# Optimization experiments

Hardware: AMD Instinct MI355X
Metric: run time of the kernel (lower is better)

Reference implementation:

```python
import jax, jax.numpy as jnp
import numpy as np

B, S, V, D, H, F, GH, NC, L = 64, 256, 50000, 1024, 16, 4096, 100, 7, 4
DH = D // H


def _ln(x, g, b):
    m = x.mean(-1, keepdims=True)
    v = x.var(-1, keepdims=True)
    return (x - m) / jnp.sqrt(v + 1e-5) * g + b


def setup_inputs() -> dict:
    key = jax.random.key(0)
    ks = iter(jax.random.split(key, 40))
    nrm = lambda shp, s=0.02: jax.random.normal(next(ks), shp, jnp.float32) * s
    inp = {}
    inp["src"] = jax.random.randint(next(ks), (B, S), 0, V)
    inp["em_seq"] = jax.random.normal(next(ks), (B, S, 7), jnp.float32)
    inp["d_ids"] = jax.random.randint(next(ks), (B, 1), 0, B)
    inp["ut_len"] = jax.random.randint(next(ks), (B,), 1, S + 1)
    inp["emb"] = jax.random.uniform(next(ks), (V, D), jnp.float32, -0.1, 0.1)
    inp["Wqkv"] = nrm((L, 3 * D, D)); inp["bqkv"] = jnp.zeros((L, 3 * D), jnp.float32)
    inp["Wo"] = nrm((L, D, D)); inp["bo"] = jnp.zeros((L, D), jnp.float32)
    inp["W1"] = nrm((L, F, D)); inp["b1"] = jnp.zeros((L, F), jnp.float32)
    inp["W2"] = nrm((L, D, F)); inp["b2"] = jnp.zeros((L, D), jnp.float32)
    inp["ln1_g"] = jnp.ones((L, D), jnp.float32); inp["ln1_b"] = jnp.zeros((L, D), jnp.float32)
    inp["ln2_g"] = jnp.ones((L, D), jnp.float32); inp["ln2_b"] = jnp.zeros((L, D), jnp.float32)
    inp["gru_Wih"] = nrm((3 * GH, 7), 0.1); inp["gru_Whh"] = nrm((3 * GH, GH), 0.1)
    inp["gru_bih"] = jnp.zeros((3 * GH,), jnp.float32); inp["gru_bhh"] = jnp.zeros((3 * GH,), jnp.float32)
    inp["dec_W"] = jax.random.uniform(next(ks), (NC, 2 * D + GH), jnp.float32, -0.1, 0.1)
    inp["dec_b"] = jnp.zeros((NC,), jnp.float32)
    return inp


def reference(src, em_seq, d_ids, ut_len, emb, Wqkv, bqkv, Wo, bo, W1, b1, W2, b2,
              ln1_g, ln1_b, ln2_g, ln2_b, gru_Wih, gru_Whh, gru_bih, gru_bhh,
              dec_W, dec_b):
    # embedding + scale + sinusoidal positional encoding
    x = emb[src] * jnp.sqrt(jnp.float32(D))                      # [B,S,D]
    pos = jnp.arange(S, dtype=jnp.float32)[:, None]
    div = jnp.exp(jnp.arange(0, D, 2, dtype=jnp.float32) * (-jnp.log(10000.0) / D))
    pe = jnp.stack([jnp.sin(pos * div), jnp.cos(pos * div)], -1).reshape(S, D)
    x = x + pe

    causal = jnp.tril(jnp.ones((S, S), bool))
    neg = jnp.finfo(x.dtype).min
    for l in range(L):  # post-norm transformer encoder layers (PyTorch default)
        qkv = x @ Wqkv[l].T + bqkv[l]
        q, k, v = jnp.split(qkv, 3, -1)
        q = q.reshape(B, S, H, DH); k = k.reshape(B, S, H, DH); v = v.reshape(B, S, H, DH)
        sc = jnp.einsum('bqhd,bkhd->bhqk', q, k) / jnp.sqrt(jnp.float32(DH))
        sc = jnp.where(causal, sc, neg)
        a = jax.nn.softmax(sc, -1)
        o = jnp.einsum('bhqk,bkhd->bqhd', a, v).reshape(B, S, D)
        x = _ln(x + o @ Wo[l].T + bo[l], ln1_g[l], ln1_b[l])
        ff = jax.nn.relu(x @ W1[l].T + b1[l]) @ W2[l].T + b2[l]
        x = _ln(x + ff, ln2_g[l], ln2_b[l])

    # emotion GRU (PyTorch GRU equations), scan over time
    xp = jnp.einsum('bsf,gf->sbg', em_seq, gru_Wih) + gru_bih    # [S,B,3*GH]

    def step(h, xt):
        hp = h @ gru_Whh.T + gru_bhh
        xr, xz, xn = jnp.split(xt, 3, -1)
        hr, hz, hn = jnp.split(hp, 3, -1)
        r = jax.nn.sigmoid(xr + hr)
        z = jax.nn.sigmoid(xz + hz)
        n = jnp.tanh(xn + r * hn)
        h = (1.0 - z) * n + z * h
        return h, h

    _, hs = jax.lax.scan(step, jnp.zeros((B, GH), x.dtype), xp)
    emo = hs.transpose(1, 0, 2)                                  # [B,S,GH]

    # ragged gather of the 'main' utterance per dialogue + broadcast-concat
    lens = ut_len[d_ids[:, 0]]                                   # [B]
    main = x[jnp.arange(B), lens - 1]                            # [B,D]
    pair = jnp.concatenate([x, jnp.broadcast_to(main[:, None, :], (B, S, D))], -1)
    valid = (jnp.arange(S)[None, :] < lens[:, None])[..., None]
    pair = jnp.where(valid, pair, 0.0)                           # zeros beyond ut_len, as in torch loop
    dec_ip = jnp.concatenate([pair, emo], -1)                    # [B,S,2D+GH]
    return dec_ip @ dec_W.T + dec_b                              # [B,S,NC]
```

## Files before the change

kernel.cpp:

```cpp
#include <hip/hip_runtime.h>
#include <hip/hip_bf16.h>
#include <math.h>

#define BB 64
#define SS 256
#define DD 1024
#define HH 16
#define FFN 4096
#define GHH 100
#define NCC 7
#define LL 4
#define TT (BB*SS)
#define DHH 64

typedef unsigned short u16;
typedef unsigned int u32;
typedef __attribute__((ext_vector_type(4))) float f32x4;
typedef __attribute__((ext_vector_type(8))) short s16x8;
typedef __attribute__((ext_vector_type(4))) unsigned short u16x4;

__device__ __forceinline__ u16 f2bf(float f) {
  union { float f; u32 u; } x; x.f = f;
  u32 r = x.u + 0x7FFFu + ((x.u >> 16) & 1u);
  return (u16)(r >> 16);
}
__device__ __forceinline__ float bf2f(u16 b) {
  union { u32 u; float f; } x; x.u = ((u32)b) << 16;
  return x.f;
}

__global__ void k_f2bf4(const float* __restrict__ s0, u16* __restrict__ d0, int n0,
                        const float* __restrict__ s1, u16* __restrict__ d1, int n1,
                        const float* __restrict__ s2, u16* __restrict__ d2, int n2,
                        const float* __restrict__ s3, u16* __restrict__ d3, int n3) {
  int stride = gridDim.x * blockDim.x;
  int total = n0 + n1 + n2 + n3;
  for (int i = blockIdx.x * blockDim.x + threadIdx.x; i < total; i += stride) {
    const float* s; u16* d; int j = i;
    if (j < n0) { s = s0; d = d0; }
    else {
      j -= n0;
      if (j < n1) { s = s1; d = d1; }
      else {
        j -= n1;
        if (j < n2) { s = s2; d = d2; }
        else { j -= n2; s = s3; d = d3; }
      }
    }
    f32x4 v = *(const f32x4*)(s + (size_t)j * 4);
    u16x4 o;
    o[0] = f2bf(v[0]); o[1] = f2bf(v[1]); o[2] = f2bf(v[2]); o[3] = f2bf(v[3]);
    *(u16x4*)(d + (size_t)j * 4) = o;
  }
}

__global__ void k_pe(float* __restrict__ pe) {
  int i = blockIdx.x * blockDim.x + threadIdx.x;
  if (i >= SS * DD / 2) return;
  int s = i / (DD / 2), j = i % (DD / 2);
  float div = __expf((float)(2 * j) * (-9.210340371976184f / (float)DD));
  float a = (float)s * div;
  pe[s * DD + 2 * j]     = sinf(a);
  pe[s * DD + 2 * j + 1] = cosf(a);
}

__global__ void k_embed(const int* __restrict__ src, const float* __restrict__ emb,
                        const float* __restrict__ pe, float* __restrict__ x32,
                        u16* __restrict__ xb) {
  int i = blockIdx.x * blockDim.x + threadIdx.x;
  if (i >= TT * DD / 4) return;
  int t = i / (DD / 4);
  int d4 = (i % (DD / 4)) * 4;
  int s = t % SS;
  int tok = src[t];
  f32x4 e = *(const f32x4*)(emb + (size_t)tok * DD + d4);
  f32x4 p = *(const f32x4*)(pe + (size_t)s * DD + d4);
  f32x4 r;
  r[0] = e[0] * 32.0f + p[0]; r[1] = e[1] * 32.0f + p[1];
  r[2] = e[2] * 32.0f + p[2]; r[3] = e[3] * 32.0f + p[3];
  *(f32x4*)(x32 + (size_t)t * DD + d4) = r;
  u16x4 o;
  o[0] = f2bf(r[0]); o[1] = f2bf(r[1]); o[2] = f2bf(r[2]); o[3] = f2bf(r[3]);
  *(u16x4*)(xb + (size_t)t * DD + d4) = o;
}

#define MEMF asm volatile("" ::: "memory")
#define GBAR do { MEMF; __builtin_amdgcn_sched_barrier(0); __builtin_amdgcn_s_barrier(); __builtin_amdgcn_sched_barrier(0); MEMF; } while(0)
#define VMW4 asm volatile("s_waitcnt vmcnt(4)" ::: "memory")

#define STG(P, isB, h, l, buf, kt) \
  __builtin_amdgcn_global_load_lds( \
    (const __attribute__((address_space(1))) u32*)(P[h][l] + (kt)), \
    (__attribute__((address_space(3))) u32*)(smem + (buf)*65536 + (isB)*32768 + (h)*16384 + (l)*8192 + wid*1024), \
    16, 0, 0)

#define LDB(buf) do { \
  _Pragma("unroll") for (int nf = 0; nf < 4; nf++) \
  _Pragma("unroll") for (int kk = 0; kk < 2; kk++) { \
    int rel = (wn*64 + nf*16 + lm)*128 + kk*64 + lg*16; \
    bq[nf][kk] = *(const s16x8*)(smem + (buf)*65536 + 32768 + (rel ^ (((rel>>9)&1)<<5))); \
  } } while(0)

#define LDA(buf, q) do { \
  _Pragma("unroll") for (int ml = 0; ml < 2; ml++) \
  _Pragma("unroll") for (int kk = 0; kk < 2; kk++) { \
    int rel = (wm*128 + ((q)*2+ml)*16 + lm)*128 + kk*64 + lg*16; \
    aq[ml][kk] = *(const s16x8*)(smem + (buf)*65536 + (rel ^ (((rel>>9)&1)<<5))); \
  } } while(0)

#define MFMAQ(q) do { \
  __builtin_amdgcn_s_setprio(1); \
  _Pragma("unroll") for (int ml = 0; ml < 2; ml++) \
  _Pragma("unroll") for (int nf = 0; nf < 4; nf++) \
  _Pragma("unroll") for (int kk = 0; kk < 2; kk++) \
    acc[(q)*2+ml][nf] = __builtin_amdgcn_mfma_f32_16x16x32_bf16(aq[ml][kk], bq[nf][kk], acc[(q)*2+ml][nf], 0, 0, 0); \
  __builtin_amdgcn_s_setprio(0); \
} while(0)

template<int EPI>
__global__ __launch_bounds__(512, 2)
void k_gemm256(const u16* __restrict__ A, const u16* __restrict__ W,
               const float* __restrict__ bias, u16* __restrict__ C,
               int M, int N, int K) {
  extern __shared__ char smem[];
  const int tid = threadIdx.x;
  const int lane = tid & 63;
  const int wid = tid >> 6;
  const int lm = lane & 15, lg = lane >> 4;
  const int wm = wid >> 2, wn = wid & 3;

  const int NB = N >> 8;
  const int nwg = gridDim.x;
  const int bid = blockIdx.x;
  const int cpx = nwg >> 3;
  const int swzb = (bid & 7) * cpx + (bid >> 3);
  const int m0 = (swzb / NB) << 8;
  const int n0 = (swzb % NB) << 8;

  const u16* pA[2][2];
  const u16* pB[2][2];
#pragma unroll
  for (int h = 0; h < 2; h++)
#pragma unroll
    for (int l = 0; l < 2; l++) {
      int rel = h * 16384 + l * 8192 + tid * 16;
      int sb = rel ^ (((rel >> 9) & 1) << 5);
      int grow = sb >> 7;
      int gcol = (sb & 127) >> 1;
      pA[h][l] = A + (size_t)(m0 + grow) * K + gcol;
      pB[h][l] = W + (size_t)(n0 + grow) * K + gcol;
    }

  f32x4 acc[8][4];
#pragma unroll
  for (int i = 0; i < 8; i++)
#pragma unroll
    for (int j = 0; j < 4; j++) acc[i][j] = (f32x4){0.f, 0.f, 0.f, 0.f};

  s16x8 bq[4][2];
  s16x8 aq[2][2];

  const int NT = K >> 6;

  STG(pB,1,0,0,0,0); STG(pB,1,0,1,0,0); STG(pB,1,1,0,0,0); STG(pB,1,1,1,0,0);
  STG(pA,0,0,0,0,0); STG(pA,0,0,1,0,0); STG(pA,0,1,0,0,0); STG(pA,0,1,1,0,0);
  STG(pB,1,0,0,1,64); STG(pB,1,0,1,1,64); STG(pB,1,1,0,1,64); STG(pB,1,1,1,1,64);
  VMW4;
  GBAR;

  for (int i = 0; i < (NT >> 1); i++) {
    const int t1k = (2*i + 1) * 64;
    int t2 = 2*i + 2; if (t2 >= NT) t2 -= NT;
    int t3 = 2*i + 3; if (t3 >= NT) t3 -= NT;
    const int t2k = t2 * 64, t3k = t3 * 64;

    LDB(0); LDA(0,0);
    STG(pA,0,0,0,1,t1k); STG(pA,0,0,1,1,t1k);
    GBAR; MFMAQ(0); GBAR;
    LDA(0,1);
    STG(pA,0,1,0,1,t1k); STG(pA,0,1,1,1,t1k);
    STG(pB,1,0,0,0,t2k); STG(pB,1,0,1,0,t2k);
    GBAR; MFMAQ(1); GBAR;
    LDA(0,2);
    STG(pB,1,1,0,0,t2k); STG(pB,1,1,1,0,t2k);
    GBAR; MFMAQ(2); GBAR;
    LDA(0,3);
    GBAR; MFMAQ(3); VMW4; GBAR;
    LDB(1); LDA(1,0);
    STG(pA,0,0,0,0,t2k); STG(pA,0,0,1,0,t2k);
    GBAR; MFMAQ(0); GBAR;
    LDA(1,1);
    STG(pA,0,1,0,0,t2k); STG(pA,0,1,1,0,t2k);
    GBAR; MFMAQ(1); GBAR;
    LDA(1,2);
    STG(pB,1,0,0,1,t3k); STG(pB,1,0,1,1,t3k);
    GBAR; MFMAQ(2); GBAR;
    LDA(1,3);
    STG(pB,1,1,0,1,t3k); STG(pB,1,1,1,1,t3k);
    GBAR; MFMAQ(3); VMW4; GBAR;
  }

  float bn[4];
#pragma unroll
  for (int nf = 0; nf < 4; nf++) bn[nf] = bias[n0 + wn*64 + nf*16 + lm];
#pragma unroll
  for (int mf = 0; mf < 8; mf++)
#pragma unroll
    for (int nf = 0; nf < 4; nf++) {
      int col = n0 + wn*64 + nf*16 + lm;
#pragma unroll
      for (int r = 0; r < 4; r++) {
        int row = m0 + wm*128 + mf*16 + lg*4 + r;
        float v = acc[mf][nf][r] + bn[nf];
        if (EPI == 1) v = fmaxf(v, 0.f);
        C[(size_t)row * N + col] = f2bf(v);
      }
    }
}

__global__ __launch_bounds__(256, 2)
void k_attn(const u16* __restrict__ qkv, u16* __restrict__ o) {
  const int h = blockIdx.x;
  const int b = blockIdx.y;
  const int lane = threadIdx.x & 63;
  const int w = threadIdx.x >> 6;
  const int lm = lane & 15, lg = lane >> 4;

  __shared__ u16 Ks[64 * 64];
  __shared__ u16 Vt[64 * 64];
  __shared__ u16 Ps[4][64 * 64];

  const size_t tokbase = (size_t)b * SS;

  s16x8 aq[4][2];
#pragma unroll
  for (int mf = 0; mf < 4; mf++) {
    const u16* qrow = qkv + (tokbase + w * 64 + mf * 16 + lm) * 3072 + h * 64;
#pragma unroll
    for (int kk = 0; kk < 2; kk++)
      aq[mf][kk] = *(const s16x8*)(qrow + kk * 32 + lg * 8);
  }

  f32x4 zero = {0.f, 0.f, 0.f, 0.f};
  f32x4 oacc[4][4];
#pragma unroll
  for (int mf = 0; mf < 4; mf++)
#pragma unroll
    for (int df = 0; df < 4; df++) oacc[mf][df] = zero;
  float m_run[16], l_run[16];
#pragma unroll
  for (int r = 0; r < 16; r++) { m_run[r] = -3e38f; l_run[r] = 0.f; }

  for (int kb = 0; kb < 4; kb++) {
    __syncthreads();
    {
      int krow = threadIdx.x >> 2;
      int seg  = (threadIdx.x & 3) * 16;
      const u16* ksrc = qkv + (tokbase + kb * 64 + krow) * 3072 + 1024 + h * 64 + seg;
      s16x8 v0 = *(const s16x8*)(ksrc);
      s16x8 v1 = *(const s16x8*)(ksrc + 8);
      *(s16x8*)&Ks[krow * 64 + seg] = v0;
      *(s16x8*)&Ks[krow * 64 + seg + 8] = v1;
      const u16* vsrc = qkv + (tokbase + kb * 64 + krow) * 3072 + 2048 + h * 64 + seg;
      s16x8 w0 = *(const s16x8*)(vsrc);
      s16x8 w1 = *(const s16x8*)(vsrc + 8);
#pragma unroll
      for (int e = 0; e < 8; e++) {
        Vt[(seg + e) * 64 + krow]     = (u16)w0[e];
        Vt[(seg + 8 + e) * 64 + krow] = (u16)w1[e];
      }
    }
    __syncthreads();
    if (w < kb) continue;

    s16x8 bk[4][2];
#pragma unroll
    for (int nf = 0; nf < 4; nf++)
#pragma unroll
      for (int kk = 0; kk < 2; kk++)
        bk[nf][kk] = *(const s16x8*)&Ks[(nf * 16 + lm) * 64 + kk * 32 + lg * 8];

    const int colbase = kb * 64;
#pragma unroll
    for (int mf = 0; mf < 4; mf++) {
      f32x4 sfr[4];
#pragma unroll
      for (int nf = 0; nf < 4; nf++) {
        f32x4 acc = zero;
#pragma unroll
        for (int kk = 0; kk < 2; kk++)
          acc = __builtin_amdgcn_mfma_f32_16x16x32_bf16(aq[mf][kk], bk[nf][kk], acc, 0, 0, 0);
        sfr[nf] = acc;
      }
      const int rowbase = w * 64 + mf * 16 + lg * 4;
#pragma unroll
      for (int nf = 0; nf < 4; nf++) {
        int col = colbase + nf * 16 + lm;
#pragma unroll
        for (int r = 0; r < 4; r++) {
          float v = sfr[nf][r] * 0.125f;
          sfr[nf][r] = (col <= rowbase + r) ? v : -1e30f;
        }
      }
#pragma unroll
      for (int r = 0; r < 4; r++) {
        float m = fmaxf(fmaxf(sfr[0][r], sfr[1][r]), fmaxf(sfr[2][r], sfr[3][r]));
#pragma unroll
        for (int off = 1; off < 16; off <<= 1) m = fmaxf(m, __shfl_xor(m, off));
        int idx = mf * 4 + r;
        float mnew = fmaxf(m_run[idx], m);
        float fo = __expf(m_run[idx] - mnew);
        m_run[idx] = mnew;
        float ps = 0.f;
#pragma unroll
        for (int nf = 0; nf < 4; nf++) {
          float p = __expf(sfr[nf][r] - mnew);
          sfr[nf][r] = p;
          ps += p;
        }
#pragma unroll
        for (int off = 1; off < 16; off <<= 1) ps += __shfl_xor(ps, off);
        l_run[idx] = l_run[idx] * fo + ps;
#pragma unroll
        for (int df = 0; df < 4; df++) oacc[mf][df][r] *= fo;
      }
#pragma unroll
      for (int nf = 0; nf < 4; nf++)
#pragma unroll
        for (int r = 0; r < 4; r++)
          Ps[w][(mf * 16 + lg * 4 + r) * 64 + nf * 16 + lm] = f2bf(sfr[nf][r]);
    }
    asm volatile("" ::: "memory");
    s16x8 bv[4][2];
#pragma unroll
    for (int df = 0; df < 4; df++)
#pragma unroll
      for (int kk = 0; kk < 2; kk++)
        bv[df][kk] = *(const s16x8*)&Vt[(df * 16 + lm) * 64 + kk * 32 + lg * 8];
#pragma unroll
    for (int mf = 0; mf < 4; mf++) {
      s16x8 pa[2];
#pragma unroll
      for (int kk = 0; kk < 2; kk++)
        pa[kk] = *(const s16x8*)&Ps[w][(mf * 16 + lm) * 64 + kk * 32 + lg * 8];
#pragma unroll
      for (int df = 0; df < 4; df++)
#pragma unroll
        for (int kk = 0; kk < 2; kk++)
          oacc[mf][df] = __builtin_amdgcn_mfma_f32_16x16x32_bf16(pa[kk], bv[df][kk], oacc[mf][df], 0, 0, 0);
    }
  }

#pragma unroll
  for (int mf = 0; mf < 4; mf++)
#pragma unroll
    for (int df = 0; df < 4; df++)
#pragma unroll
      for (int r = 0; r < 4; r++) {
        int row = w * 64 + mf * 16 + lg * 4 + r;
        float val = oacc[mf][df][r] / l_run[mf * 4 + r];
        o[(tokbase + row) * 1024 + h * 64 + df * 16 + lm] = f2bf(val);
      }
}

__global__ __launch_bounds__(256)
void k_ln(const float* __restrict__ xin, const u16* __restrict__ tmp,
          const float* __restrict__ gam, const float* __restrict__ bet,
          float* __restrict__ xout, u16* __restrict__ xb) {
  int t = blockIdx.x;
  int tid = threadIdx.x;
  f32x4 v = *(const f32x4*)(xin + (size_t)t * DD + tid * 4);
  u16x4 u4 = *(const u16x4*)(tmp + (size_t)t * DD + tid * 4);
  v[0] += bf2f(u4[0]); v[1] += bf2f(u4[1]); v[2] += bf2f(u4[2]); v[3] += bf2f(u4[3]);
  float s = v[0] + v[1] + v[2] + v[3];
  float s2 = v[0]*v[0] + v[1]*v[1] + v[2]*v[2] + v[3]*v[3];
#pragma unroll
  for (int off = 32; off >= 1; off >>= 1) {
    s  += __shfl_xor(s, off);
    s2 += __shfl_xor(s2, off);
  }
  __shared__ float red[8];
  int w = tid >> 6;
  if ((tid & 63) == 0) { red[w] = s; red[4 + w] = s2; }
  __syncthreads();
  s  = red[0] + red[1] + red[2] + red[3];
  s2 = red[4] + red[5] + red[6] + red[7];
  float mean = s * (1.f / 1024.f);
  float var = s2 * (1.f / 1024.f) - mean * mean;
  float rstd = rsqrtf(var + 1e-5f);
  f32x4 g4 = *(const f32x4*)(gam + tid * 4);
  f32x4 b4 = *(const f32x4*)(bet + tid * 4);
  f32x4 y;
  u16x4 yo;
#pragma unroll
  for (int e = 0; e < 4; e++) {
    y[e] = (v[e] - mean) * rstd * g4[e] + b4[e];
    yo[e] = f2bf(y[e]);
  }
  *(f32x4*)(xout + (size_t)t * DD + tid * 4) = y;
  *(u16x4*)(xb + (size_t)t * DD + tid * 4) = yo;
}

__global__ __launch_bounds__(256, 1)
void k_gru(const float* __restrict__ em, const float* __restrict__ Wih,
           const float* __restrict__ bih, const float* __restrict__ Whh,
           const float* __restrict__ bhh, float* __restrict__ emo) {
  const int b = blockIdx.x;
  const int tid = threadIdx.x;
  const int iraw = tid >> 1;
  const int i = iraw < 100 ? iraw : 99;
  const bool act = iraw < 100;
  const int half = tid & 1;
  __shared__ __align__(16) float h[2][104];

  f32x4 wr[13], wz[13], wn[13];
#pragma unroll
  for (int q = 0; q < 13; q++) {
#pragma unroll
    for (int e4 = 0; e4 < 4; e4++) {
      int k = q * 4 + e4;
      int kk = half * 50 + (k < 50 ? k : 0);
      float vr = Whh[(size_t)i * 100 + kk];
      float vz = Whh[(size_t)(100 + i) * 100 + kk];
      float vn = Whh[(size_t)(200 + i) * 100 + kk];
      wr[q][e4] = (k < 50) ? vr : 0.f;
      wz[q][e4] = (k < 50) ? vz : 0.f;
      wn[q][e4] = (k < 50) ? vn : 0.f;
    }
  }
  float wir[7], wiz[7], win[7];
#pragma unroll
  for (int f = 0; f < 7; f++) {
    wir[f] = Wih[i * 7 + f];
    wiz[f] = Wih[(100 + i) * 7 + f];
    win[f] = Wih[(200 + i) * 7 + f];
  }
  const float br = bhh[i], bz = bhh[100 + i], bn = bhh[200 + i];
  const float xbr = bih[i], xbz = bih[100 + i], xbn = bih[200 + i];

  if (tid < 104) { h[0][tid] = 0.f; h[1][tid] = 0.f; }
  __syncthreads();

  const float* eb = em + (size_t)b * SS * 7;
  float e[7];
#pragma unroll
  for (int f = 0; f < 7; f++) e[f] = eb[f];

  for (int s = 0; s < SS; ++s) {
    const int cur = s & 1, nxt = cur ^ 1;
    float sr = xbr, sz = xbz, sn = xbn;
#pragma unroll
    for (int f = 0; f < 7; f++) {
      sr += wir[f] * e[f]; sz += wiz[f] * e[f]; sn += win[f] * e[f];
    }
    {
      int sp = (s + 1 < SS) ? s + 1 : s;
#pragma unroll
      for (int f = 0; f < 7; f++) e[f] = eb[sp * 7 + f];
    }
    const float* hb = &h[cur][half * 52];
    f32x4 ac_r = {0.f,0.f,0.f,0.f}, ac_z = {0.f,0.f,0.f,0.f}, ac_n = {0.f,0.f,0.f,0.f};
#pragma unroll
    for (int q = 0; q < 13; q++) {
      f32x4 hv = *(const f32x4*)(hb + q * 4);
      ac_r += wr[q] * hv;
      ac_z += wz[q] * hv;
      ac_n += wn[q] * hv;
    }
    float ar = (ac_r[0] + ac_r[1]) + (ac_r[2] + ac_r[3]);
    float az = (ac_z[0] + ac_z[1]) + (ac_z[2] + ac_z[3]);
    float an = (ac_n[0] + ac_n[1]) + (ac_n[2] + ac_n[3]);
    ar += __shfl_xor(ar, 1);
    az += __shfl_xor(az, 1);
    an += __shfl_xor(an, 1);
    if (act && half == 0) {
      int slot = i + (i >= 50 ? 2 : 0);
      float hold = h[cur][slot];
      float rr = 1.f / (1.f + __expf(-(sr + ar + br)));
      float zz = 1.f / (1.f + __expf(-(sz + az + bz)));
      float nx = sn + rr * (an + bn);
      float e2 = __expf(-2.f * fabsf(nx));
      float th = (1.f - e2) / (1.f + e2);
      float nn = copysignf(th, nx);
      float hn = (1.f - zz) * nn + zz * hold;
      h[nxt][slot] = hn;
      emo[((size_t)b * SS + s) * GHH + i] = hn;
    }
    __syncthreads();
  }
}

__global__ void k_main(const int* __restrict__ d_ids, const int* __restrict__ ut_len,
                       const float* __restrict__ x32, const float* __restrict__ decW,
                       float* __restrict__ md) {
  int b = blockIdx.x;
  int lane = threadIdx.x;
  int len = ut_len[d_ids[b]];
  const float* xr = x32 + ((size_t)b * SS + (len - 1)) * DD;
  float acc[NCC];
#pragma unroll
  for (int c = 0; c < NCC; c++) acc[c] = 0.f;
  for (int d = lane; d < DD; d += 64) {
    float xv = xr[d];
#pragma unroll
    for (int c = 0; c < NCC; c++) acc[c] += xv * decW[(size_t)c * 2148 + 1024 + d];
  }
#pragma unroll
  for (int c = 0; c < NCC; c++) {
#pragma unroll
    for (int off = 32; off >= 1; off >>= 1) acc[c] += __shfl_xor(acc[c], off);
  }
  if (lane == 0) {
#pragma unroll
    for (int c = 0; c < NCC; c++) md[b * NCC + c] = acc[c];
  }
}

__global__ __launch_bounds__(256)
void k_dec(const float* __restrict__ x32, const float* __restrict__ emo,
           const float* __restrict__ md, const float* __restrict__ decW,
           const float* __restrict__ decb, const int* __restrict__ d_ids,
           const int* __restrict__ ut_len, float* __restrict__ out) {
  int grp = threadIdx.x >> 6, lane = threadIdx.x & 63;
  int t = blockIdx.x * 4 + grp;
  int b = t / SS, s = t % SS;
  int len = ut_len[d_ids[b]];
  bool valid = s < len;
  float acc[NCC];
#pragma unroll
  for (int c = 0; c < NCC; c++) acc[c] = 0.f;
  if (valid) {
    const float* xr = x32 + (size_t)t * DD;
    for (int d = lane; d < DD; d += 64) {
      float xv = xr[d];
#pragma unroll
      for (int c = 0; c < NCC; c++) acc[c] += xv * decW[(size_t)c * 2148 + d];
    }
  }
  {
    const float* er = emo + (size_t)t * GHH;
    for (int d = lane; d < GHH; d += 64) {
      float ev = er[d];
#pragma unroll
      for (int c = 0; c < NCC; c++) acc[c] += ev * decW[(size_t)c * 2148 + 2048 + d];
    }
  }
#pragma unroll
  for (int c = 0; c < NCC; c++) {
#pragma unroll
    for (int off = 32; off >= 1; off >>= 1) acc[c] += __shfl_xor(acc[c], off);
  }
  if (lane == 0) {
#pragma unroll
    for (int c = 0; c < NCC; c++) {
      float v = acc[c] + (valid ? md[b * NCC + c] : 0.f) + decb[c];
      out[(size_t)t * NCC + c] = v;
    }
  }
}

extern "C" void kernel_launch(void* const* d_in, const int* in_sizes, int n_in,
                              void* d_out, int out_size, void* d_ws, size_t ws_size,
                              hipStream_t stream) {
  const int*   src    = (const int*)d_in[0];
  const float* em_seq = (const float*)d_in[1];
  const int*   d_ids  = (const int*)d_in[2];
  const int*   ut_len = (const int*)d_in[3];
  const float* emb    = (const float*)d_in[4];
  const float* Wqkv   = (const float*)d_in[5];
  const float* bqkv   = (const float*)d_in[6];
  const float* Wo     = (const float*)d_in[7];
  const float* bo     = (const float*)d_in[8];
  const float* W1     = (const float*)d_in[9];
  const float* b1     = (const float*)d_in[10];
  const float* W2     = (const float*)d_in[11];
  const float* b2     = (const float*)d_in[12];
  const float* ln1g   = (const float*)d_in[13];
  const float* ln1b   = (const float*)d_in[14];
  const float* ln2g   = (const float*)d_in[15];
  const float* ln2b   = (const float*)d_in[16];
  const float* gWih   = (const float*)d_in[17];
  const float* gWhh   = (const float*)d_in[18];
  const float* gbih   = (const float*)d_in[19];
  const float* gbhh   = (const float*)d_in[20];
  const float* decW   = (const float*)d_in[21];
  const float* decb   = (const float*)d_in[22];
  float* out = (float*)d_out;

  char* wsp = (char*)d_ws;
  auto take = [&](size_t n) { char* p = wsp; wsp += (n + 255) & ~(size_t)255; return p; };

  u16*   wqkvb = (u16*)take((size_t)3072 * 1024 * 2);
  u16*   wob   = (u16*)take((size_t)1024 * 1024 * 2);
  u16*   w1b   = (u16*)take((size_t)4096 * 1024 * 2);
  u16*   w2b   = (u16*)take((size_t)1024 * 4096 * 2);
  float* pe    = (float*)take((size_t)SS * DD * 4);
  float* x32   = (float*)take((size_t)TT * DD * 4);
  u16*   xb    = (u16*)take((size_t)TT * DD * 2);
  u16*   big   = (u16*)take((size_t)TT * FFN * 2);
  u16*   ob    = (u16*)take((size_t)TT * DD * 2);
  u16*   tmp16 = (u16*)take((size_t)TT * DD * 2);
  float* emo   = (float*)take((size_t)BB * SS * GHH * 4);
  float* md    = (float*)take((size_t)BB * NCC * 4);

  (void)hipFuncSetAttribute((const void*)&k_gemm256<0>,
      hipFuncAttributeMaxDynamicSharedMemorySize, 131072);
  (void)hipFuncSetAttribute((const void*)&k_gemm256<1>,
      hipFuncAttributeMaxDynamicSharedMemorySize, 131072);

  k_gru<<<BB, 256, 0, stream>>>(em_seq, gWih, gbih, gWhh, gbhh, emo);

  k_pe<<<(SS * DD / 2 + 255) / 256, 256, 0, stream>>>(pe);
  k_embed<<<TT * DD / 4 / 256, 256, 0, stream>>>(src, emb, pe, x32, xb);

  for (int l = 0; l < LL; ++l) {
    k_f2bf4<<<2048, 256, 0, stream>>>(
        Wqkv + (size_t)l * 3072 * 1024, wqkvb, 3072 * 1024 / 4,
        Wo   + (size_t)l * 1024 * 1024, wob,   1024 * 1024 / 4,
        W1   + (size_t)l * 4096 * 1024, w1b,   4096 * 1024 / 4,
        W2   + (size_t)l * 1024 * 4096, w2b,   1024 * 4096 / 4);

    k_gemm256<0><<<(TT/256) * (3072/256), 512, 131072, stream>>>(
        xb, wqkvb, bqkv + (size_t)l * 3072, big, TT, 3072, 1024);
    k_attn<<<dim3(HH, BB), 256, 0, stream>>>(big, ob);
    k_gemm256<0><<<(TT/256) * (1024/256), 512, 131072, stream>>>(
        ob, wob, bo + (size_t)l * 1024, tmp16, TT, 1024, 1024);
    k_ln<<<TT, 256, 0, stream>>>(x32, tmp16, ln1g + (size_t)l * DD, ln1b + (size_t)l * DD, x32, xb);
    k_gemm256<1><<<(TT/256) * (4096/256), 512, 131072, stream>>>(
        xb, w1b, b1 + (size_t)l * 4096, big, TT, 4096, 1024);
    k_gemm256<0><<<(TT/256) * (1024/256), 512, 131072, stream>>>(
        big, w2b, b2 + (size_t)l * 1024, tmp16, TT, 1024, 4096);
    k_ln<<<TT, 256, 0, stream>>>(x32, tmp16, ln2g + (size_t)l * DD, ln2b + (size_t)l * DD, x32, xb);
  }

  k_main<<<BB, 64, 0, stream>>>(d_ids, ut_len, x32, decW, md);
  k_dec<<<TT / 4, 256, 0, stream>>>(x32, emo, md, decW, decb, d_ids, ut_len, out);
}
```

Baseline: 2.469 ms.

## Drop fp32 residual stream, keep activations only in bf16; unroll GRU weights into scalars

Removes the fp32 copy of the hidden state (x32) and carries the residual stream only in bf16, so embed, layernorm and the decoder read and write half the bytes and skip an extra write per token. LayerNorm now reads the bf16 residual and overwrites it in place. The GRU kernel's weight arrays are replaced with macro-expanded named registers, which helps keep them out of scratch memory. The trade-off is lower residual precision across layers, which may push outputs past tolerance.

```diff
diff --git a/kernel.cpp b/kernel.cpp
--- a/kernel.cpp
+++ b/kernel.cpp
@@ -65,8 +65,7 @@
 }
 
 __global__ void k_embed(const int* __restrict__ src, const float* __restrict__ emb,
-                        const float* __restrict__ pe, float* __restrict__ x32,
-                        u16* __restrict__ xb) {
+                        const float* __restrict__ pe, u16* __restrict__ xb) {
   int i = blockIdx.x * blockDim.x + threadIdx.x;
   if (i >= TT * DD / 4) return;
   int t = i / (DD / 4);
@@ -75,12 +74,9 @@
   int tok = src[t];
   f32x4 e = *(const f32x4*)(emb + (size_t)tok * DD + d4);
   f32x4 p = *(const f32x4*)(pe + (size_t)s * DD + d4);
-  f32x4 r;
-  r[0] = e[0] * 32.0f + p[0]; r[1] = e[1] * 32.0f + p[1];
-  r[2] = e[2] * 32.0f + p[2]; r[3] = e[3] * 32.0f + p[3];
-  *(f32x4*)(x32 + (size_t)t * DD + d4) = r;
   u16x4 o;
-  o[0] = f2bf(r[0]); o[1] = f2bf(r[1]); o[2] = f2bf(r[2]); o[3] = f2bf(r[3]);
+  o[0] = f2bf(e[0] * 32.0f + p[0]); o[1] = f2bf(e[1] * 32.0f + p[1]);
+  o[2] = f2bf(e[2] * 32.0f + p[2]); o[3] = f2bf(e[3] * 32.0f + p[3]);
   *(u16x4*)(xb + (size_t)t * DD + d4) = o;
 }
 
@@ -364,14 +360,15 @@
 }
 
 __global__ __launch_bounds__(256)
-void k_ln(const float* __restrict__ xin, const u16* __restrict__ tmp,
-          const float* __restrict__ gam, const float* __restrict__ bet,
-          float* __restrict__ xout, u16* __restrict__ xb) {
+void k_ln(u16* __restrict__ xb, const u16* __restrict__ tmp,
+          const float* __restrict__ gam, const float* __restrict__ bet) {
   int t = blockIdx.x;
   int tid = threadIdx.x;
-  f32x4 v = *(const f32x4*)(xin + (size_t)t * DD + tid * 4);
+  u16x4 a4 = *(const u16x4*)(xb + (size_t)t * DD + tid * 4);
   u16x4 u4 = *(const u16x4*)(tmp + (size_t)t * DD + tid * 4);
-  v[0] += bf2f(u4[0]); v[1] += bf2f(u4[1]); v[2] += bf2f(u4[2]); v[3] += bf2f(u4[3]);
+  f32x4 v;
+#pragma unroll
+  for (int e = 0; e < 4; e++) v[e] = bf2f(a4[e]) + bf2f(u4[e]);
   float s = v[0] + v[1] + v[2] + v[3];
   float s2 = v[0]*v[0] + v[1]*v[1] + v[2]*v[2] + v[3]*v[3];
 #pragma unroll
@@ -390,16 +387,15 @@
   float rstd = rsqrtf(var + 1e-5f);
   f32x4 g4 = *(const f32x4*)(gam + tid * 4);
   f32x4 b4 = *(const f32x4*)(bet + tid * 4);
-  f32x4 y;
   u16x4 yo;
 #pragma unroll
-  for (int e = 0; e < 4; e++) {
-    y[e] = (v[e] - mean) * rstd * g4[e] + b4[e];
-    yo[e] = f2bf(y[e]);
-  }
-  *(f32x4*)(xout + (size_t)t * DD + tid * 4) = y;
+  for (int e = 0; e < 4; e++)
+    yo[e] = f2bf((v[e] - mean) * rstd * g4[e] + b4[e]);
   *(u16x4*)(xb + (size_t)t * DD + tid * 4) = yo;
 }
+
+#define QL(X) X(0) X(1) X(2) X(3) X(4) X(5) X(6) X(7) X(8) X(9) X(10) X(11)
+#define F7(X) X(0) X(1) X(2) X(3) X(4) X(5) X(6)
 
 __global__ __launch_bounds__(256, 1)
 void k_gru(const float* __restrict__ em, const float* __restrict__ Wih,
@@ -413,28 +409,26 @@
   const int half = tid & 1;
   __shared__ __align__(16) float h[2][104];
 
-  f32x4 wr[13], wz[13], wn[13];
-#pragma unroll
-  for (int q = 0; q < 13; q++) {
-#pragma unroll
-    for (int e4 = 0; e4 < 4; e4++) {
-      int k = q * 4 + e4;
-      int kk = half * 50 + (k < 50 ? k : 0);
-      float vr = Whh[(size_t)i * 100 + kk];
-      float vz = Whh[(size_t)(100 + i) * 100 + kk];
-      float vn = Whh[(size_t)(200 + i) * 100 + kk];
-      wr[q][e4] = (k < 50) ? vr : 0.f;
-      wz[q][e4] = (k < 50) ? vz : 0.f;
-      wn[q][e4] = (k < 50) ? vn : 0.f;
-    }
-  }
-  float wir[7], wiz[7], win[7];
-#pragma unroll
-  for (int f = 0; f < 7; f++) {
-    wir[f] = Wih[i * 7 + f];
-    wiz[f] = Wih[(100 + i) * 7 + f];
-    win[f] = Wih[(200 + i) * 7 + f];
-  }
+  const float* rowR = Whh + (size_t)i * 100 + half * 50;
+  const float* rowZ = Whh + (size_t)(100 + i) * 100 + half * 50;
+  const float* rowN = Whh + (size_t)(200 + i) * 100 + half * 50;
+
+#define LOADQ(q) \
+  f32x4 wr##q = {rowR[4*q], rowR[4*q+1], rowR[4*q+2], rowR[4*q+3]}; \
+  f32x4 wz##q = {rowZ[4*q], rowZ[4*q+1], rowZ[4*q+2], rowZ[4*q+3]}; \
+  f32x4 wn##q = {rowN[4*q], rowN[4*q+1], rowN[4*q+2], rowN[4*q+3]};
+  QL(LOADQ)
+#undef LOADQ
+  f32x4 wr12 = {rowR[48], rowR[49], 0.f, 0.f};
+  f32x4 wz12 = {rowZ[48], rowZ[49], 0.f, 0.f};
+  f32x4 wn12 = {rowN[48], rowN[49], 0.f, 0.f};
+
+#define LOADI(f) \
+  float wir##f = Wih[i * 7 + f]; \
+  float wiz##f = Wih[(100 + i) * 7 + f]; \
+  float win##f = Wih[(200 + i) * 7 + f];
+  F7(LOADI)
+#undef LOADI
   const float br = bhh[i], bz = bhh[100 + i], bn = bhh[200 + i];
   const float xbr = bih[i], xbz = bih[100 + i], xbn = bih[200 + i];
 
@@ -442,34 +436,31 @@
   __syncthreads();
 
   const float* eb = em + (size_t)b * SS * 7;
-  float e[7];
-#pragma unroll
-  for (int f = 0; f < 7; f++) e[f] = eb[f];
+#define DECLE(f) float e##f = eb[f];
+  F7(DECLE)
+#undef DECLE
 
   for (int s = 0; s < SS; ++s) {
     const int cur = s & 1, nxt = cur ^ 1;
     float sr = xbr, sz = xbz, sn = xbn;
-#pragma unroll
-    for (int f = 0; f < 7; f++) {
-      sr += wir[f] * e[f]; sz += wiz[f] * e[f]; sn += win[f] * e[f];
-    }
+#define MACI(f) sr += wir##f * e##f; sz += wiz##f * e##f; sn += win##f * e##f;
+    F7(MACI)
+#undef MACI
     {
       int sp = (s + 1 < SS) ? s + 1 : s;
-#pragma unroll
-      for (int f = 0; f < 7; f++) e[f] = eb[sp * 7 + f];
+#define LDE(f) e##f = eb[sp * 7 + f];
+      F7(LDE)
+#undef LDE
     }
     const float* hb = &h[cur][half * 52];
-    f32x4 ac_r = {0.f,0.f,0.f,0.f}, ac_z = {0.f,0.f,0.f,0.f}, ac_n = {0.f,0.f,0.f,0.f};
-#pragma unroll
-    for (int q = 0; q < 13; q++) {
-      f32x4 hv = *(const f32x4*)(hb + q * 4);
-      ac_r += wr[q] * hv;
-      ac_z += wz[q] * hv;
-      ac_n += wn[q] * hv;
-    }
-    float ar = (ac_r[0] + ac_r[1]) + (ac_r[2] + ac_r[3]);
-    float az = (ac_z[0] + ac_z[1]) + (ac_z[2] + ac_z[3]);
-    float an = (ac_n[0] + ac_n[1]) + (ac_n[2] + ac_n[3]);
+    f32x4 ar4 = {0.f,0.f,0.f,0.f}, az4 = {0.f,0.f,0.f,0.f}, an4 = {0.f,0.f,0.f,0.f};
+#define MACQ(q) { f32x4 hv = *(const f32x4*)(hb + 4*q); \
+    ar4 += wr##q * hv; az4 += wz##q * hv; an4 += wn##q * hv; }
+    QL(MACQ) MACQ(12)
+#undef MACQ
+    float ar = (ar4[0] + ar4[1]) + (ar4[2] + ar4[3]);
+    float az = (az4[0] + az4[1]) + (az4[2] + az4[3]);
+    float an = (an4[0] + an4[1]) + (an4[2] + an4[3]);
     ar += __shfl_xor(ar, 1);
     az += __shfl_xor(az, 1);
     an += __shfl_xor(an, 1);
@@ -491,17 +482,17 @@
 }
 
 __global__ void k_main(const int* __restrict__ d_ids, const int* __restrict__ ut_len,
-                       const float* __restrict__ x32, const float* __restrict__ decW,
+                       const u16* __restrict__ x, const float* __restrict__ decW,
                        float* __restrict__ md) {
   int b = blockIdx.x;
   int lane = threadIdx.x;
   int len = ut_len[d_ids[b]];
-  const float* xr = x32 + ((size_t)b * SS + (len - 1)) * DD;
+  const u16* xr = x + ((size_t)b * SS + (len - 1)) * DD;
   float acc[NCC];
 #pragma unroll
   for (int c = 0; c < NCC; c++) acc[c] = 0.f;
   for (int d = lane; d < DD; d += 64) {
-    float xv = xr[d];
+    float xv = bf2f(xr[d]);
 #pragma unroll
     for (int c = 0; c < NCC; c++) acc[c] += xv * decW[(size_t)c * 2148 + 1024 + d];
   }
@@ -517,7 +508,7 @@
 }
 
 __global__ __launch_bounds__(256)
-void k_dec(const float* __restrict__ x32, const float* __restrict__ emo,
+void k_dec(const u16* __restrict__ x, const float* __restrict__ emo,
            const float* __restrict__ md, const float* __restrict__ decW,
            const float* __restrict__ decb, const int* __restrict__ d_ids,
            const int* __restrict__ ut_len, float* __restrict__ out) {
@@ -530,9 +521,9 @@
 #pragma unroll
   for (int c = 0; c < NCC; c++) acc[c] = 0.f;
   if (valid) {
-    const float* xr = x32 + (size_t)t * DD;
+    const u16* xrow = x + (size_t)t * DD;
     for (int d = lane; d < DD; d += 64) {
-      float xv = xr[d];
+      float xv = bf2f(xrow[d]);
 #pragma unroll
       for (int c = 0; c < NCC; c++) acc[c] += xv * decW[(size_t)c * 2148 + d];
     }
@@ -595,7 +586,6 @@
   u16*   w1b   = (u16*)take((size_t)4096 * 1024 * 2);
   u16*   w2b   = (u16*)take((size_t)1024 * 4096 * 2);
   float* pe    = (float*)take((size_t)SS * DD * 4);
-  float* x32   = (float*)take((size_t)TT * DD * 4);
   u16*   xb    = (u16*)take((size_t)TT * DD * 2);
   u16*   big   = (u16*)take((size_t)TT * FFN * 2);
   u16*   ob    = (u16*)take((size_t)TT * DD * 2);
@@ -611,7 +601,7 @@
   k_gru<<<BB, 256, 0, stream>>>(em_seq, gWih, gbih, gWhh, gbhh, emo);
 
   k_pe<<<(SS * DD / 2 + 255) / 256, 256, 0, stream>>>(pe);
-  k_embed<<<TT * DD / 4 / 256, 256, 0, stream>>>(src, emb, pe, x32, xb);
+  k_embed<<<TT * DD / 4 / 256, 256, 0, stream>>>(src, emb, pe, xb);
 
   for (int l = 0; l < LL; ++l) {
     k_f2bf4<<<2048, 256, 0, stream>>>(
@@ -625,14 +615,14 @@
     k_attn<<<dim3(HH, BB), 256, 0, stream>>>(big, ob);
     k_gemm256<0><<<(TT/256) * (1024/256), 512, 131072, stream>>>(
         ob, wob, bo + (size_t)l * 1024, tmp16, TT, 1024, 1024);
-    k_ln<<<TT, 256, 0, stream>>>(x32, tmp16, ln1g + (size_t)l * DD, ln1b + (size_t)l * DD, x32, xb);
+    k_ln<<<TT, 256, 0, stream>>>(xb, tmp16, ln1g + (size_t)l * DD, ln1b + (size_t)l * DD);
     k_gemm256<1><<<(TT/256) * (4096/256), 512, 131072, stream>>>(
         xb, w1b, b1 + (size_t)l * 4096, big, TT, 4096, 1024);
     k_gemm256<0><<<(TT/256) * (1024/256), 512, 131072, stream>>>(
         big, w2b, b2 + (size_t)l * 1024, tmp16, TT, 1024, 4096);
-    k_ln<<<TT, 256, 0, stream>>>(x32, tmp16, ln2g + (size_t)l * DD, ln2b + (size_t)l * DD, x32, xb);
-  }
-
-  k_main<<<BB, 64, 0, stream>>>(d_ids, ut_len, x32, decW, md);
-  k_dec<<<TT / 4, 256, 0, stream>>>(x32, emo, md, decW, decb, d_ids, ut_len, out);
-}
+    k_ln<<<TT, 256, 0, stream>>>(xb, tmp16, ln2g + (size_t)l * DD, ln2b + (size_t)l * DD);
+  }
+
+  k_main<<<BB, 64, 0, stream>>>(d_ids, ut_len, xb, decW, md);
+  k_dec<<<TT / 4, 256, 0, stream>>>(xb, emo, md, decW, decb, d_ids, ut_len, out);
+}
```

New measurement: 2.324 ms. 5.9% less time.
